# Optimization experiments

Measured on AMD Instinct MI355X. Metric: run time of the kernel, lower is better.

Reference implementation:

```python
import jax, jax.numpy as jnp
import numpy as np

T = 512          # num_frames
IN_DIM = 85      # pose+beta feature dim
HID = 1024       # hidden_dim
LAYERS = 3       # num_stacks
VERTS = 6890     # SMPL mesh vertices


def _lstm_layer(x_seq, W_ih, W_hh, b_ih, b_hh):
    """Single-layer LSTM over time, batch=1 (PyTorch gate order i,f,g,o).
    x_seq: [T, in_dim] -> hs: [T, HID]"""
    h0 = jnp.zeros((HID,), dtype=x_seq.dtype)
    c0 = jnp.zeros((HID,), dtype=x_seq.dtype)
    # precompute input contributions for all timesteps in one GEMM: [T, 4H]
    x_gates = x_seq @ W_ih.T + (b_ih + b_hh)

    def step(carry, xg):
        h, c = carry
        gates = xg + W_hh @ h          # [4H]
        i, f, g, o = jnp.split(gates, 4)
        i = jax.nn.sigmoid(i)
        f = jax.nn.sigmoid(f)
        g = jnp.tanh(g)
        o = jax.nn.sigmoid(o)
        c = f * c + i * g
        h = o * jnp.tanh(c)
        return (h, c), h

    (_, _), hs = jax.lax.scan(step, (h0, c0), x_gates)
    return hs


def setup_inputs() -> dict:
    key = jax.random.key(0)
    ks = jax.random.split(key, 4 * LAYERS + 2)
    inp = {"pose_beta_seq": jax.random.normal(ks[0], (T, IN_DIM), dtype=jnp.float32)}
    s = 1.0 / np.sqrt(HID)  # PyTorch uniform(-1/sqrt(h), 1/sqrt(h)) init scale
    ki = 1
    for l in range(LAYERS):
        in_dim = IN_DIM if l == 0 else HID
        inp[f"W_ih_{l}"] = jax.random.uniform(ks[ki + 0], (4 * HID, in_dim), minval=-s, maxval=s, dtype=jnp.float32)
        inp[f"W_hh_{l}"] = jax.random.uniform(ks[ki + 1], (4 * HID, HID), minval=-s, maxval=s, dtype=jnp.float32)
        inp[f"b_ih_{l}"] = jax.random.uniform(ks[ki + 2], (4 * HID,), minval=-s, maxval=s, dtype=jnp.float32)
        inp[f"b_hh_{l}"] = jax.random.uniform(ks[ki + 3], (4 * HID,), minval=-s, maxval=s, dtype=jnp.float32)
        ki += 4
    inp["W_out"] = jax.random.uniform(ks[ki], (VERTS * 3, HID), minval=-s, maxval=s, dtype=jnp.float32)
    return inp


def reference(pose_beta_seq, W_ih_0, W_hh_0, b_ih_0, b_hh_0,
              W_ih_1, W_hh_1, b_ih_1, b_hh_1,
              W_ih_2, W_hh_2, b_ih_2, b_hh_2, W_out):
    layers = [(W_ih_0, W_hh_0, b_ih_0, b_hh_0),
              (W_ih_1, W_hh_1, b_ih_1, b_hh_1),
              (W_ih_2, W_hh_2, b_ih_2, b_hh_2)]
    h = pose_beta_seq
    for (Wih, Whh, bih, bhh) in layers:
        h = _lstm_layer(h, Wih, Whh, bih, bhh)
    dbs = (h @ W_out.T).reshape(T, VERTS, 3)
    return dbs
```

## Files before the change

### kernel.cpp

```cpp
#include <hip/hip_runtime.h>
#include <stdint.h>

#define TT    512
#define HID   1024
#define G4    4096
#define INDIM 85
#define NOUT  20670

typedef unsigned long long u64;

__global__ __launch_bounds__(256)
void gemm_nt(const float* __restrict__ A, const float* __restrict__ B,
             const float* __restrict__ bias0, const float* __restrict__ bias1,
             float* __restrict__ C, int M, int N, int K)
{
    __shared__ float As[16 * 68];
    __shared__ float Bs[16 * 68];
    const int tid = threadIdx.x;
    const int tx = tid & 15, ty = tid >> 4;
    const int m0 = blockIdx.y * 64, n0 = blockIdx.x * 64;
    float acc[4][4] = {};
    const int KT = (K + 15) >> 4;

    for (int kt = 0; kt < KT; ++kt) {
        const int k0 = kt << 4;
        __syncthreads();
        for (int l = tid; l < 1024; l += 256) {
            const int mm = l >> 4, kk = l & 15;
            const int kg = k0 + kk;
            As[kk * 68 + mm] = (kg < K) ? A[(size_t)(m0 + mm) * K + kg] : 0.f;
            Bs[kk * 68 + mm] = (kg < K && (n0 + mm) < N)
                                   ? B[(size_t)(n0 + mm) * K + kg] : 0.f;
        }
        __syncthreads();
        #pragma unroll
        for (int kk = 0; kk < 16; ++kk) {
            const float4 av = *(const float4*)&As[kk * 68 + ty * 4];
            const float4 bv = *(const float4*)&Bs[kk * 68 + tx * 4];
            const float a[4] = {av.x, av.y, av.z, av.w};
            const float b[4] = {bv.x, bv.y, bv.z, bv.w};
            #pragma unroll
            for (int i = 0; i < 4; ++i)
                #pragma unroll
                for (int j = 0; j < 4; ++j)
                    acc[i][j] += a[i] * b[j];
        }
    }

    float bj[4];
    #pragma unroll
    for (int j = 0; j < 4; ++j) {
        const int n = n0 + tx * 4 + j;
        float bv = 0.f;
        if (n < N) {
            if (bias0) bv += bias0[n];
            if (bias1) bv += bias1[n];
        }
        bj[j] = bv;
    }
    #pragma unroll
    for (int i = 0; i < 4; ++i) {
        const int m = m0 + ty * 4 + i;
        #pragma unroll
        for (int j = 0; j < 4; ++j) {
            const int n = n0 + tx * 4 + j;
            if (n < N) C[(size_t)m * N + n] = acc[i][j] + bj[j];
        }
    }
}

__device__ __forceinline__ float sig_(float x) { return 1.f / (1.f + expf(-x)); }

__global__ __launch_bounds__(256, 3)
void lstm_fused(const float* __restrict__ xg,
                const float* __restrict__ Whh0,
                const float* __restrict__ Wih1, const float* __restrict__ Whh1,
                const float* __restrict__ bih1, const float* __restrict__ bhh1,
                const float* __restrict__ Wih2, const float* __restrict__ Whh2,
                const float* __restrict__ bih2, const float* __restrict__ bhh2,
                u64* __restrict__ hbuf0, u64* __restrict__ hbuf1,
                u64* __restrict__ hbuf2, float* __restrict__ hs2)
{
    __shared__ float hin_lds[HID];
    __shared__ float hprev_lds[HID];
    __shared__ float gsum[4][4];

    const int tid = threadIdx.x;
    const int w = tid >> 6, ln = tid & 63, q = ln & 31;
    const bool inHalf = (ln < 32);
    const int layer = blockIdx.x >> 8;
    const int b = blockIdx.x & 255;
    const int u0 = 4 * b;
    const int unit = u0 + w;

    const float* Wih = (layer == 1) ? Wih1 : Wih2;
    const float* Whh = (layer == 0) ? Whh0 : (layer == 1 ? Whh1 : Whh2);
    u64* hbI = (layer == 1) ? hbuf0 : hbuf1;
    u64* hbP = (layer == 0) ? hbuf0 : (layer == 1 ? hbuf1 : hbuf2);

    float4 Wv[4][8];
    if (layer == 0 && inHalf) {
        #pragma unroll
        for (int g = 0; g < 4; ++g)
            #pragma unroll
            for (int j = 0; j < 8; ++j)
                Wv[g][j] = make_float4(0.f, 0.f, 0.f, 0.f);
    } else {
        const float* M = inHalf ? Wih : Whh;
        #pragma unroll
        for (int g = 0; g < 4; ++g) {
            const float* rp = M + (size_t)(g * HID + unit) * HID + 4 * q;
            #pragma unroll
            for (int j = 0; j < 8; ++j)
                Wv[g][j] = *(const float4*)(rp + 128 * j);
        }
    }

    float add4[4] = {0.f, 0.f, 0.f, 0.f};
    if (w == 0 && ln < 4 && layer > 0) {
        #pragma unroll
        for (int g = 0; g < 4; ++g) {
            const int r = g * HID + u0 + ln;
            add4[g] = (layer == 1) ? (bih1[r] + bhh1[r]) : (bih2[r] + bhh2[r]);
        }
    }

    if (layer == 0) {
        const int p4z = 4 * ((tid + b) & 255);
        *(float4*)&hin_lds[p4z] = make_float4(0.f, 0.f, 0.f, 0.f);
    }

    float c = 0.f;
    for (int t = 0; t < TT; ++t) {
        if (layer == 0 && w == 0 && ln < 4) {
            #pragma unroll
            for (int g = 0; g < 4; ++g)
                add4[g] = xg[(size_t)t * G4 + g * HID + u0 + ln];
        }

        const int p4 = 4 * ((tid + b) & 255);
        bool doneP = (t == 0), doneI = (layer == 0);
        u64 vp0 = 0, vp1 = 0, vp2 = 0, vp3 = 0;
        u64 vi0 = 0, vi1 = 0, vi2 = 0, vi3 = 0;
        const u64 tagP = (u64)(unsigned)t;
        const u64 tagI = (u64)(unsigned)(t + 1);
        const u64* pp = hbP + (size_t)(t - 1) * HID + p4;
        const u64* pi = hbI + (size_t)t * HID + p4;
        int guard = 0;
        for (;;) {
            if (!doneP) {
                vp0 = __hip_atomic_load(pp + 0, __ATOMIC_RELAXED, __HIP_MEMORY_SCOPE_AGENT);
                if ((vp0 >> 32) == tagP) {
                    vp1 = __hip_atomic_load(pp + 1, __ATOMIC_RELAXED, __HIP_MEMORY_SCOPE_AGENT);
                    vp2 = __hip_atomic_load(pp + 2, __ATOMIC_RELAXED, __HIP_MEMORY_SCOPE_AGENT);
                    vp3 = __hip_atomic_load(pp + 3, __ATOMIC_RELAXED, __HIP_MEMORY_SCOPE_AGENT);
                    doneP = (vp1 >> 32) == tagP && (vp2 >> 32) == tagP &&
                            (vp3 >> 32) == tagP;
                }
            }
            if (!doneI) {
                vi0 = __hip_atomic_load(pi + 0, __ATOMIC_RELAXED, __HIP_MEMORY_SCOPE_AGENT);
                if ((vi0 >> 32) == tagI) {
                    vi1 = __hip_atomic_load(pi + 1, __ATOMIC_RELAXED, __HIP_MEMORY_SCOPE_AGENT);
                    vi2 = __hip_atomic_load(pi + 2, __ATOMIC_RELAXED, __HIP_MEMORY_SCOPE_AGENT);
                    vi3 = __hip_atomic_load(pi + 3, __ATOMIC_RELAXED, __HIP_MEMORY_SCOPE_AGENT);
                    doneI = (vi1 >> 32) == tagI && (vi2 >> 32) == tagI &&
                            (vi3 >> 32) == tagI;
                }
            }
            if (doneP && doneI) break;
            if (++guard > (1 << 22)) break;
            __builtin_amdgcn_s_sleep(1);
        }
        if (t == 0)
            *(float4*)&hprev_lds[p4] = make_float4(0.f, 0.f, 0.f, 0.f);
        else
            *(float4*)&hprev_lds[p4] = make_float4(
                __uint_as_float((unsigned)vp0), __uint_as_float((unsigned)vp1),
                __uint_as_float((unsigned)vp2), __uint_as_float((unsigned)vp3));
        if (layer > 0)
            *(float4*)&hin_lds[p4] = make_float4(
                __uint_as_float((unsigned)vi0), __uint_as_float((unsigned)vi1),
                __uint_as_float((unsigned)vi2), __uint_as_float((unsigned)vi3));
        __syncthreads();

        const float* hsrc = (inHalf ? hin_lds : hprev_lds) + 4 * q;
        float a0 = 0.f, a1 = 0.f, a2 = 0.f, a3 = 0.f;
        #pragma unroll
        for (int j = 0; j < 8; ++j) {
            const float4 hv = *(const float4*)(hsrc + 128 * j);
            a0 += Wv[0][j].x * hv.x + Wv[0][j].y * hv.y + Wv[0][j].z * hv.z + Wv[0][j].w * hv.w;
            a1 += Wv[1][j].x * hv.x + Wv[1][j].y * hv.y + Wv[1][j].z * hv.z + Wv[1][j].w * hv.w;
            a2 += Wv[2][j].x * hv.x + Wv[2][j].y * hv.y + Wv[2][j].z * hv.z + Wv[2][j].w * hv.w;
            a3 += Wv[3][j].x * hv.x + Wv[3][j].y * hv.y + Wv[3][j].z * hv.z + Wv[3][j].w * hv.w;
        }
        #pragma unroll
        for (int off = 1; off < 64; off <<= 1) {
            a0 += __shfl_xor(a0, off, 64);
            a1 += __shfl_xor(a1, off, 64);
            a2 += __shfl_xor(a2, off, 64);
            a3 += __shfl_xor(a3, off, 64);
        }
        if (ln == 0) {
            gsum[w][0] = a0; gsum[w][1] = a1; gsum[w][2] = a2; gsum[w][3] = a3;
        }
        __syncthreads();

        if (w == 0 && ln < 4) {
            const float i_ = sig_(gsum[ln][0] + add4[0]);
            const float f_ = sig_(gsum[ln][1] + add4[1]);
            const float g_ = tanhf(gsum[ln][2] + add4[2]);
            const float o_ = sig_(gsum[ln][3] + add4[3]);
            c = f_ * c + i_ * g_;
            const float h = o_ * tanhf(c);
            if (layer == 2) hs2[(size_t)t * HID + u0 + ln] = h;
            const u64 pv = (((u64)(unsigned)(t + 1)) << 32) |
                           (u64)__float_as_uint(h);
            __hip_atomic_store(hbP + (size_t)t * HID + u0 + ln, pv,
                               __ATOMIC_RELAXED, __HIP_MEMORY_SCOPE_AGENT);
        }
    }
}

extern "C" void kernel_launch(void* const* d_in, const int* in_sizes, int n_in,
                              void* d_out, int out_size, void* d_ws, size_t ws_size,
                              hipStream_t stream)
{
    (void)in_sizes; (void)n_in; (void)out_size; (void)ws_size;

    const float* pose = (const float*)d_in[0];
    const float* Wih0 = (const float*)d_in[1];
    const float* Whh0 = (const float*)d_in[2];
    const float* bih0 = (const float*)d_in[3];
    const float* bhh0 = (const float*)d_in[4];
    const float* Wih1 = (const float*)d_in[5];
    const float* Whh1 = (const float*)d_in[6];
    const float* bih1 = (const float*)d_in[7];
    const float* bhh1 = (const float*)d_in[8];
    const float* Wih2 = (const float*)d_in[9];
    const float* Whh2 = (const float*)d_in[10];
    const float* bih2 = (const float*)d_in[11];
    const float* bhh2 = (const float*)d_in[12];
    const float* Wout = (const float*)d_in[13];
    float* out = (float*)d_out;

    char* ws = (char*)d_ws;
    const size_t HB = (size_t)TT * HID * sizeof(u64);
    u64* hbuf0 = (u64*)ws;
    u64* hbuf1 = (u64*)(ws + HB);
    u64* hbuf2 = (u64*)(ws + 2 * HB);
    float* xg  = (float*)(ws + 3 * HB);
    float* hs2 = (float*)(ws + 3 * HB + (size_t)TT * G4 * sizeof(float));

    hipMemsetAsync(hbuf0, 0, 3 * HB, stream);

    const dim3 blk(256);
    gemm_nt<<<dim3(G4 / 64, TT / 64), blk, 0, stream>>>(
        pose, Wih0, bih0, bhh0, xg, TT, G4, INDIM);
    lstm_fused<<<dim3(768), blk, 0, stream>>>(
        xg, Whh0, Wih1, Whh1, bih1, bhh1, Wih2, Whh2, bih2, bhh2,
        hbuf0, hbuf1, hbuf2, hs2);
    gemm_nt<<<dim3((NOUT + 63) / 64, TT / 64), blk, 0, stream>>>(
        hs2, Wout, nullptr, nullptr, out, TT, NOUT, HID);
}
```

Before: 4.724 ms.

## Batch input-to-hidden projection in 32-step chunks inside fused LSTM kernel

```diff
diff --git a/kernel.cpp b/kernel.cpp
--- a/kernel.cpp
+++ b/kernel.cpp
@@ -6,6 +6,7 @@
 #define G4    4096
 #define INDIM 85
 #define NOUT  20670
+#define CHK   32
 
 typedef unsigned long long u64;
 
@@ -81,57 +82,111 @@
                 u64* __restrict__ hbuf0, u64* __restrict__ hbuf1,
                 u64* __restrict__ hbuf2, float* __restrict__ hs2)
 {
-    __shared__ float hin_lds[HID];
     __shared__ float hprev_lds[HID];
     __shared__ float gsum[4][4];
+    __shared__ float xgbuf[CHK][4][4];
+    __shared__ float Wt[16][128];
+    __shared__ float Ht[32 * 129];
 
     const int tid = threadIdx.x;
-    const int w = tid >> 6, ln = tid & 63, q = ln & 31;
-    const bool inHalf = (ln < 32);
+    const int w = tid >> 6, ln = tid & 63;
     const int layer = blockIdx.x >> 8;
     const int b = blockIdx.x & 255;
     const int u0 = 4 * b;
     const int unit = u0 + w;
 
+    const float* Whh = (layer == 0) ? Whh0 : (layer == 1 ? Whh1 : Whh2);
     const float* Wih = (layer == 1) ? Wih1 : Wih2;
-    const float* Whh = (layer == 0) ? Whh0 : (layer == 1 ? Whh1 : Whh2);
     u64* hbI = (layer == 1) ? hbuf0 : hbuf1;
     u64* hbP = (layer == 0) ? hbuf0 : (layer == 1 ? hbuf1 : hbuf2);
 
-    float4 Wv[4][8];
-    if (layer == 0 && inHalf) {
+    float Wv[4][16];
+    #pragma unroll
+    for (int g = 0; g < 4; ++g) {
+        const float* rp = Whh + (size_t)(g * HID + unit) * HID + ln;
+        #pragma unroll
+        for (int j = 0; j < 16; ++j)
+            Wv[g][j] = rp[64 * j];
+    }
+
+    float bias4[4] = {0.f, 0.f, 0.f, 0.f};
+    if (layer == 1) {
         #pragma unroll
         for (int g = 0; g < 4; ++g)
-            #pragma unroll
-            for (int j = 0; j < 8; ++j)
-                Wv[g][j] = make_float4(0.f, 0.f, 0.f, 0.f);
-    } else {
-        const float* M = inHalf ? Wih : Whh;
-        #pragma unroll
-        for (int g = 0; g < 4; ++g) {
-            const float* rp = M + (size_t)(g * HID + unit) * HID + 4 * q;
-            #pragma unroll
-            for (int j = 0; j < 8; ++j)
-                Wv[g][j] = *(const float4*)(rp + 128 * j);
-        }
-    }
-
-    float add4[4] = {0.f, 0.f, 0.f, 0.f};
-    if (w == 0 && ln < 4 && layer > 0) {
-        #pragma unroll
-        for (int g = 0; g < 4; ++g) {
-            const int r = g * HID + u0 + ln;
-            add4[g] = (layer == 1) ? (bih1[r] + bhh1[r]) : (bih2[r] + bhh2[r]);
-        }
-    }
-
-    if (layer == 0) {
-        const int p4z = 4 * ((tid + b) & 255);
-        *(float4*)&hin_lds[p4z] = make_float4(0.f, 0.f, 0.f, 0.f);
+            bias4[g] = bih1[g * HID + unit] + bhh1[g * HID + unit];
+    } else if (layer == 2) {
+        #pragma unroll
+        for (int g = 0; g < 4; ++g)
+            bias4[g] = bih2[g * HID + unit] + bhh2[g * HID + unit];
     }
 
     float c = 0.f;
     for (int t = 0; t < TT; ++t) {
+        if (layer > 0 && (t & (CHK - 1)) == 0) {
+            const int tc = ln & 31, half = ln >> 5;
+            float acc[4];
+            #pragma unroll
+            for (int g = 0; g < 4; ++g) acc[g] = (half == 0) ? bias4[g] : 0.f;
+
+            const int wr = tid >> 4;
+            const int wc = (tid & 15) * 8;
+            const float* wsrc = Wih + (size_t)((wr >> 2) * HID + u0 + (wr & 3)) * HID + wc;
+            const int stc = tid >> 3;
+            const int skk = (tid & 7) * 16;
+
+            for (int kt = 0; kt < 8; ++kt) {
+                __syncthreads();
+                *(float4*)&Wt[wr][wc]     = *(const float4*)(wsrc + kt * 128);
+                *(float4*)&Wt[wr][wc + 4] = *(const float4*)(wsrc + kt * 128 + 4);
+                {
+                    const u64* src = hbI + (size_t)(t + stc) * HID + kt * 128 + skk;
+                    const u64 tag = (u64)(unsigned)(t + stc + 1);
+                    u64 v[16];
+                    int guard = 0;
+                    for (;;) {
+                        bool ok = true;
+                        #pragma unroll
+                        for (int i = 0; i < 16; ++i)
+                            v[i] = __hip_atomic_load(src + i, __ATOMIC_RELAXED,
+                                                     __HIP_MEMORY_SCOPE_AGENT);
+                        #pragma unroll
+                        for (int i = 0; i < 16; ++i)
+                            ok = ok && ((v[i] >> 32) == tag);
+                        if (ok) break;
+                        if (++guard > (1 << 22)) break;
+                        __builtin_amdgcn_s_sleep(1);
+                    }
+                    float* hrow = &Ht[stc * 129 + skk];
+                    #pragma unroll
+                    for (int i = 0; i < 16; ++i)
+                        hrow[i] = __uint_as_float((unsigned)v[i]);
+                }
+                __syncthreads();
+                const float* hrow = &Ht[tc * 129 + half * 64];
+                #pragma unroll
+                for (int kb = 0; kb < 16; ++kb) {
+                    const float h0 = hrow[kb * 4 + 0];
+                    const float h1 = hrow[kb * 4 + 1];
+                    const float h2 = hrow[kb * 4 + 2];
+                    const float h3 = hrow[kb * 4 + 3];
+                    #pragma unroll
+                    for (int g = 0; g < 4; ++g) {
+                        const float4 w4 = *(const float4*)&Wt[g * 4 + w][half * 64 + kb * 4];
+                        acc[g] += w4.x * h0 + w4.y * h1 + w4.z * h2 + w4.w * h3;
+                    }
+                }
+            }
+            #pragma unroll
+            for (int g = 0; g < 4; ++g)
+                acc[g] += __shfl_xor(acc[g], 32, 64);
+            if (ln < 32) {
+                #pragma unroll
+                for (int g = 0; g < 4; ++g)
+                    xgbuf[tc][w][g] = acc[g];
+            }
+        }
+
+        float add4[4];
         if (layer == 0 && w == 0 && ln < 4) {
             #pragma unroll
             for (int g = 0; g < 4; ++g)
@@ -139,60 +194,40 @@
         }
 
         const int p4 = 4 * ((tid + b) & 255);
-        bool doneP = (t == 0), doneI = (layer == 0);
-        u64 vp0 = 0, vp1 = 0, vp2 = 0, vp3 = 0;
-        u64 vi0 = 0, vi1 = 0, vi2 = 0, vi3 = 0;
-        const u64 tagP = (u64)(unsigned)t;
-        const u64 tagI = (u64)(unsigned)(t + 1);
-        const u64* pp = hbP + (size_t)(t - 1) * HID + p4;
-        const u64* pi = hbI + (size_t)t * HID + p4;
-        int guard = 0;
-        for (;;) {
-            if (!doneP) {
+        if (t == 0) {
+            *(float4*)&hprev_lds[p4] = make_float4(0.f, 0.f, 0.f, 0.f);
+        } else {
+            const u64 tagP = (u64)(unsigned)t;
+            const u64* pp = hbP + (size_t)(t - 1) * HID + p4;
+            u64 vp0 = 0, vp1 = 0, vp2 = 0, vp3 = 0;
+            int guard = 0;
+            for (;;) {
                 vp0 = __hip_atomic_load(pp + 0, __ATOMIC_RELAXED, __HIP_MEMORY_SCOPE_AGENT);
                 if ((vp0 >> 32) == tagP) {
                     vp1 = __hip_atomic_load(pp + 1, __ATOMIC_RELAXED, __HIP_MEMORY_SCOPE_AGENT);
                     vp2 = __hip_atomic_load(pp + 2, __ATOMIC_RELAXED, __HIP_MEMORY_SCOPE_AGENT);
                     vp3 = __hip_atomic_load(pp + 3, __ATOMIC_RELAXED, __HIP_MEMORY_SCOPE_AGENT);
-                    doneP = (vp1 >> 32) == tagP && (vp2 >> 32) == tagP &&
-                            (vp3 >> 32) == tagP;
+                    if ((vp1 >> 32) == tagP && (vp2 >> 32) == tagP &&
+                        (vp3 >> 32) == tagP)
+                        break;
                 }
+                if (++guard > (1 << 22)) break;
+                __builtin_amdgcn_s_sleep(1);
             }
-            if (!doneI) {
-                vi0 = __hip_atomic_load(pi + 0, __ATOMIC_RELAXED, __HIP_MEMORY_SCOPE_AGENT);
-                if ((vi0 >> 32) == tagI) {
-                    vi1 = __hip_atomic_load(pi + 1, __ATOMIC_RELAXED, __HIP_MEMORY_SCOPE_AGENT);
-                    vi2 = __hip_atomic_load(pi + 2, __ATOMIC_RELAXED, __HIP_MEMORY_SCOPE_AGENT);
-                    vi3 = __hip_atomic_load(pi + 3, __ATOMIC_RELAXED, __HIP_MEMORY_SCOPE_AGENT);
-                    doneI = (vi1 >> 32) == tagI && (vi2 >> 32) == tagI &&
-                            (vi3 >> 32) == tagI;
-                }
-            }
-            if (doneP && doneI) break;
-            if (++guard > (1 << 22)) break;
-            __builtin_amdgcn_s_sleep(1);
-        }
-        if (t == 0)
-            *(float4*)&hprev_lds[p4] = make_float4(0.f, 0.f, 0.f, 0.f);
-        else
             *(float4*)&hprev_lds[p4] = make_float4(
                 __uint_as_float((unsigned)vp0), __uint_as_float((unsigned)vp1),
                 __uint_as_float((unsigned)vp2), __uint_as_float((unsigned)vp3));
-        if (layer > 0)
-            *(float4*)&hin_lds[p4] = make_float4(
-                __uint_as_float((unsigned)vi0), __uint_as_float((unsigned)vi1),
-                __uint_as_float((unsigned)vi2), __uint_as_float((unsigned)vi3));
+        }
         __syncthreads();
 
-        const float* hsrc = (inHalf ? hin_lds : hprev_lds) + 4 * q;
         float a0 = 0.f, a1 = 0.f, a2 = 0.f, a3 = 0.f;
         #pragma unroll
-        for (int j = 0; j < 8; ++j) {
-            const float4 hv = *(const float4*)(hsrc + 128 * j);
-            a0 += Wv[0][j].x * hv.x + Wv[0][j].y * hv.y + Wv[0][j].z * hv.z + Wv[0][j].w * hv.w;
-            a1 += Wv[1][j].x * hv.x + Wv[1][j].y * hv.y + Wv[1][j].z * hv.z + Wv[1][j].w * hv.w;
-            a2 += Wv[2][j].x * hv.x + Wv[2][j].y * hv.y + Wv[2][j].z * hv.z + Wv[2][j].w * hv.w;
-            a3 += Wv[3][j].x * hv.x + Wv[3][j].y * hv.y + Wv[3][j].z * hv.z + Wv[3][j].w * hv.w;
+        for (int j = 0; j < 16; ++j) {
+            const float h = hprev_lds[ln + 64 * j];
+            a0 += Wv[0][j] * h;
+            a1 += Wv[1][j] * h;
+            a2 += Wv[2][j] * h;
+            a3 += Wv[3][j] * h;
         }
         #pragma unroll
         for (int off = 1; off < 64; off <<= 1) {
@@ -207,10 +242,18 @@
         __syncthreads();
 
         if (w == 0 && ln < 4) {
-            const float i_ = sig_(gsum[ln][0] + add4[0]);
-            const float f_ = sig_(gsum[ln][1] + add4[1]);
-            const float g_ = tanhf(gsum[ln][2] + add4[2]);
-            const float o_ = sig_(gsum[ln][3] + add4[3]);
+            float ad0, ad1, ad2, ad3;
+            if (layer == 0) {
+                ad0 = add4[0]; ad1 = add4[1]; ad2 = add4[2]; ad3 = add4[3];
+            } else {
+                const int tc = t & (CHK - 1);
+                ad0 = xgbuf[tc][ln][0]; ad1 = xgbuf[tc][ln][1];
+                ad2 = xgbuf[tc][ln][2]; ad3 = xgbuf[tc][ln][3];
+            }
+            const float i_ = sig_(gsum[ln][0] + ad0);
+            const float f_ = sig_(gsum[ln][1] + ad1);
+            const float g_ = tanhf(gsum[ln][2] + ad2);
+            const float o_ = sig_(gsum[ln][3] + ad3);
             c = f_ * c + i_ * g_;
             const float h = o_ * tanhf(c);
             if (layer == 2) hs2[(size_t)t * HID + u0 + ln] = h;
```

New measurement: 8.821 ms. 86.7% more time.

## Split LSTM gate dot products across two waves per unit and split polling

Applied to the files above, without the earlier changes.

```diff
diff --git a/kernel.cpp b/kernel.cpp
--- a/kernel.cpp
+++ b/kernel.cpp
@@ -8,6 +8,7 @@
 #define NOUT  20670
 
 typedef unsigned long long u64;
+typedef unsigned int u32;
 
 __global__ __launch_bounds__(256)
 void gemm_nt(const float* __restrict__ A, const float* __restrict__ B,
@@ -71,7 +72,7 @@
 
 __device__ __forceinline__ float sig_(float x) { return 1.f / (1.f + expf(-x)); }
 
-__global__ __launch_bounds__(256, 3)
+__global__ __launch_bounds__(512, 6)
 void lstm_fused(const float* __restrict__ xg,
                 const float* __restrict__ Whh0,
                 const float* __restrict__ Wih1, const float* __restrict__ Whh1,
@@ -83,36 +84,36 @@
 {
     __shared__ float hin_lds[HID];
     __shared__ float hprev_lds[HID];
-    __shared__ float gsum[4][4];
+    __shared__ float gsum[8][4];
 
     const int tid = threadIdx.x;
-    const int w = tid >> 6, ln = tid & 63, q = ln & 31;
-    const bool inHalf = (ln < 32);
+    const int w = tid >> 6, ln = tid & 63;
+    const int uloc = w >> 1, half = w & 1;
     const int layer = blockIdx.x >> 8;
     const int b = blockIdx.x & 255;
     const int u0 = 4 * b;
-    const int unit = u0 + w;
+    const int unit = u0 + uloc;
 
     const float* Wih = (layer == 1) ? Wih1 : Wih2;
     const float* Whh = (layer == 0) ? Whh0 : (layer == 1 ? Whh1 : Whh2);
     u64* hbI = (layer == 1) ? hbuf0 : hbuf1;
     u64* hbP = (layer == 0) ? hbuf0 : (layer == 1 ? hbuf1 : hbuf2);
 
-    float4 Wv[4][8];
-    if (layer == 0 && inHalf) {
+    float Wv[4][16];
+    if (half == 0 && layer == 0) {
         #pragma unroll
         for (int g = 0; g < 4; ++g)
             #pragma unroll
-            for (int j = 0; j < 8; ++j)
-                Wv[g][j] = make_float4(0.f, 0.f, 0.f, 0.f);
+            for (int j = 0; j < 16; ++j)
+                Wv[g][j] = 0.f;
     } else {
-        const float* M = inHalf ? Wih : Whh;
+        const float* M = half ? Whh : Wih;
         #pragma unroll
         for (int g = 0; g < 4; ++g) {
-            const float* rp = M + (size_t)(g * HID + unit) * HID + 4 * q;
-            #pragma unroll
-            for (int j = 0; j < 8; ++j)
-                Wv[g][j] = *(const float4*)(rp + 128 * j);
+            const float* rp = M + (size_t)(g * HID + unit) * HID + ln;
+            #pragma unroll
+            for (int j = 0; j < 16; ++j)
+                Wv[g][j] = rp[64 * j];
         }
     }
 
@@ -125,10 +126,12 @@
         }
     }
 
-    if (layer == 0) {
-        const int p4z = 4 * ((tid + b) & 255);
-        *(float4*)&hin_lds[p4z] = make_float4(0.f, 0.f, 0.f, 0.f);
-    }
+    const int sidx = tid & 255;
+    const bool isP = (tid < 256);
+    const int p4 = 4 * ((sidx + b) & 255);
+
+    if (layer == 0 && !isP)
+        *(float4*)&hin_lds[p4] = make_float4(0.f, 0.f, 0.f, 0.f);
 
     float c = 0.f;
     for (int t = 0; t < TT; ++t) {
@@ -138,61 +141,43 @@
                 add4[g] = xg[(size_t)t * G4 + g * HID + u0 + ln];
         }
 
-        const int p4 = 4 * ((tid + b) & 255);
-        bool doneP = (t == 0), doneI = (layer == 0);
-        u64 vp0 = 0, vp1 = 0, vp2 = 0, vp3 = 0;
-        u64 vi0 = 0, vi1 = 0, vi2 = 0, vi3 = 0;
-        const u64 tagP = (u64)(unsigned)t;
-        const u64 tagI = (u64)(unsigned)(t + 1);
-        const u64* pp = hbP + (size_t)(t - 1) * HID + p4;
-        const u64* pi = hbI + (size_t)t * HID + p4;
-        int guard = 0;
-        for (;;) {
-            if (!doneP) {
-                vp0 = __hip_atomic_load(pp + 0, __ATOMIC_RELAXED, __HIP_MEMORY_SCOPE_AGENT);
-                if ((vp0 >> 32) == tagP) {
-                    vp1 = __hip_atomic_load(pp + 1, __ATOMIC_RELAXED, __HIP_MEMORY_SCOPE_AGENT);
-                    vp2 = __hip_atomic_load(pp + 2, __ATOMIC_RELAXED, __HIP_MEMORY_SCOPE_AGENT);
-                    vp3 = __hip_atomic_load(pp + 3, __ATOMIC_RELAXED, __HIP_MEMORY_SCOPE_AGENT);
-                    doneP = (vp1 >> 32) == tagP && (vp2 >> 32) == tagP &&
-                            (vp3 >> 32) == tagP;
+        const bool need = isP ? (t > 0) : (layer > 0);
+        if (need) {
+            const u64* pp = isP ? (hbP + (size_t)(t - 1) * HID + p4)
+                                : (hbI + (size_t)t * HID + p4);
+            const u64 tag = isP ? (u64)(u32)t : (u64)(u32)(t + 1);
+            u64 v0 = 0, v1 = 0, v2 = 0, v3 = 0;
+            int guard = 0;
+            for (;;) {
+                v0 = __hip_atomic_load(pp + 0, __ATOMIC_RELAXED, __HIP_MEMORY_SCOPE_AGENT);
+                if ((v0 >> 32) == tag) {
+                    v1 = __hip_atomic_load(pp + 1, __ATOMIC_RELAXED, __HIP_MEMORY_SCOPE_AGENT);
+                    v2 = __hip_atomic_load(pp + 2, __ATOMIC_RELAXED, __HIP_MEMORY_SCOPE_AGENT);
+                    v3 = __hip_atomic_load(pp + 3, __ATOMIC_RELAXED, __HIP_MEMORY_SCOPE_AGENT);
+                    if ((v1 >> 32) == tag && (v2 >> 32) == tag && (v3 >> 32) == tag)
+                        break;
                 }
+                if (++guard > (1 << 18)) break;
+                __builtin_amdgcn_s_sleep(1);
             }
-            if (!doneI) {
-                vi0 = __hip_atomic_load(pi + 0, __ATOMIC_RELAXED, __HIP_MEMORY_SCOPE_AGENT);
-                if ((vi0 >> 32) == tagI) {
-                    vi1 = __hip_atomic_load(pi + 1, __ATOMIC_RELAXED, __HIP_MEMORY_SCOPE_AGENT);
-                    vi2 = __hip_atomic_load(pi + 2, __ATOMIC_RELAXED, __HIP_MEMORY_SCOPE_AGENT);
-                    vi3 = __hip_atomic_load(pi + 3, __ATOMIC_RELAXED, __HIP_MEMORY_SCOPE_AGENT);
-                    doneI = (vi1 >> 32) == tagI && (vi2 >> 32) == tagI &&
-                            (vi3 >> 32) == tagI;
-                }
-            }
-            if (doneP && doneI) break;
-            if (++guard > (1 << 22)) break;
-            __builtin_amdgcn_s_sleep(1);
-        }
-        if (t == 0)
+            float* dst = isP ? hprev_lds : hin_lds;
+            *(float4*)&dst[p4] = make_float4(
+                __uint_as_float((unsigned)v0), __uint_as_float((unsigned)v1),
+                __uint_as_float((unsigned)v2), __uint_as_float((unsigned)v3));
+        } else if (isP) {
             *(float4*)&hprev_lds[p4] = make_float4(0.f, 0.f, 0.f, 0.f);
-        else
-            *(float4*)&hprev_lds[p4] = make_float4(
-                __uint_as_float((unsigned)vp0), __uint_as_float((unsigned)vp1),
-                __uint_as_float((unsigned)vp2), __uint_as_float((unsigned)vp3));
-        if (layer > 0)
-            *(float4*)&hin_lds[p4] = make_float4(
-                __uint_as_float((unsigned)vi0), __uint_as_float((unsigned)vi1),
-                __uint_as_float((unsigned)vi2), __uint_as_float((unsigned)vi3));
-        __syncthreads();
-
-        const float* hsrc = (inHalf ? hin_lds : hprev_lds) + 4 * q;
+        }
+        __syncthreads();
+
+        const float* hsrc = half ? hprev_lds : hin_lds;
         float a0 = 0.f, a1 = 0.f, a2 = 0.f, a3 = 0.f;
         #pragma unroll
-        for (int j = 0; j < 8; ++j) {
-            const float4 hv = *(const float4*)(hsrc + 128 * j);
-            a0 += Wv[0][j].x * hv.x + Wv[0][j].y * hv.y + Wv[0][j].z * hv.z + Wv[0][j].w * hv.w;
-            a1 += Wv[1][j].x * hv.x + Wv[1][j].y * hv.y + Wv[1][j].z * hv.z + Wv[1][j].w * hv.w;
-            a2 += Wv[2][j].x * hv.x + Wv[2][j].y * hv.y + Wv[2][j].z * hv.z + Wv[2][j].w * hv.w;
-            a3 += Wv[3][j].x * hv.x + Wv[3][j].y * hv.y + Wv[3][j].z * hv.z + Wv[3][j].w * hv.w;
+        for (int j = 0; j < 16; ++j) {
+            const float h = hsrc[ln + 64 * j];
+            a0 += Wv[0][j] * h;
+            a1 += Wv[1][j] * h;
+            a2 += Wv[2][j] * h;
+            a3 += Wv[3][j] * h;
         }
         #pragma unroll
         for (int off = 1; off < 64; off <<= 1) {
@@ -207,10 +192,10 @@
         __syncthreads();
 
         if (w == 0 && ln < 4) {
-            const float i_ = sig_(gsum[ln][0] + add4[0]);
-            const float f_ = sig_(gsum[ln][1] + add4[1]);
-            const float g_ = tanhf(gsum[ln][2] + add4[2]);
-            const float o_ = sig_(gsum[ln][3] + add4[3]);
+            const float i_ = sig_(gsum[2 * ln][0] + gsum[2 * ln + 1][0] + add4[0]);
+            const float f_ = sig_(gsum[2 * ln][1] + gsum[2 * ln + 1][1] + add4[1]);
+            const float g_ = tanhf(gsum[2 * ln][2] + gsum[2 * ln + 1][2] + add4[2]);
+            const float o_ = sig_(gsum[2 * ln][3] + gsum[2 * ln + 1][3] + add4[3]);
             c = f_ * c + i_ * g_;
             const float h = o_ * tanhf(c);
             if (layer == 2) hs2[(size_t)t * HID + u0 + ln] = h;
@@ -252,14 +237,13 @@
     float* xg  = (float*)(ws + 3 * HB);
     float* hs2 = (float*)(ws + 3 * HB + (size_t)TT * G4 * sizeof(float));
 
-    hipMemsetAsync(hbuf0, 0, 3 * HB, stream);
-
-    const dim3 blk(256);
-    gemm_nt<<<dim3(G4 / 64, TT / 64), blk, 0, stream>>>(
+    (void)hipMemsetAsync(hbuf0, 0, 3 * HB, stream);
+
+    gemm_nt<<<dim3(G4 / 64, TT / 64), dim3(256), 0, stream>>>(
         pose, Wih0, bih0, bhh0, xg, TT, G4, INDIM);
-    lstm_fused<<<dim3(768), blk, 0, stream>>>(
+    lstm_fused<<<dim3(768), dim3(512), 0, stream>>>(
         xg, Whh0, Wih1, Whh1, bih1, bhh1, Wih2, Whh2, bih2, bhh2,
         hbuf0, hbuf1, hbuf2, hs2);
-    gemm_nt<<<dim3((NOUT + 63) / 64, TT / 64), blk, 0, stream>>>(
+    gemm_nt<<<dim3((NOUT + 63) / 64, TT / 64), dim3(256), 0, stream>>>(
         hs2, Wout, nullptr, nullptr, out, TT, NOUT, HID);
 }
```

Result: slower. 6.142 ms (+30.0%).
